# Optimization experiments

Hardware: AMD Instinct MI355X
Metric: run time of the kernel (lower is better)

## Reference

```python
import jax, jax.numpy as jnp
import numpy as np

HIGH, LOW = 768, 384
LOW2 = LOW // 2  # PNL uses low_dim // reduc_ratio, reduc_ratio=2
B, N = 8, 4096
EPS = 1e-5


def _nl_block(x_h, x_l, wg, bg, wt, bt, wp, bp, ww, bw, gamma, beta):
    # x_h: [B,N,H], x_l: [B,N0,H]; conv1x1 == per-token linear
    Nl = x_l.shape[1]
    g = jnp.einsum('bnc,dc->bnd', x_l, wg) + bg      # [B,N0,D]
    th = jnp.einsum('bnc,dc->bnd', x_h, wt) + bt     # [B,N,D]
    ph = jnp.einsum('bnc,dc->bnd', x_l, wp) + bp     # [B,N0,D]
    # attention = (th @ ph^T) / N0; y = attention @ g. Reassociate:
    kv = jnp.einsum('bnd,bne->bde', ph, g) / Nl      # [B,D,D]
    y = jnp.einsum('bnd,bde->bne', th, kv)           # [B,N,D]
    y = jnp.einsum('bnd,cd->bnc', y, ww) + bw        # [B,N,H]
    # BatchNorm1d over channel dim, training-mode batch stats (biased var)
    mu = y.mean(axis=(0, 1))
    var = y.var(axis=(0, 1))
    y = (y - mu) * jax.lax.rsqrt(var + EPS) * gamma + beta
    return y + x_h


def setup_inputs() -> dict:
    key = jax.random.key(0)
    ks = jax.random.split(key, 24)
    s = 0.02
    d = {
        'x': jax.random.normal(ks[0], (B, N, HIGH), jnp.float32),
        'x0': jax.random.normal(ks[1], (B, N, HIGH), jnp.float32),
        # CNL params (low_dim = 384)
        'c_wg': s * jax.random.normal(ks[2], (LOW, HIGH)), 'c_bg': s * jax.random.normal(ks[3], (LOW,)),
        'c_wt': s * jax.random.normal(ks[4], (LOW, HIGH)), 'c_bt': s * jax.random.normal(ks[5], (LOW,)),
        'c_wp': s * jax.random.normal(ks[6], (LOW, HIGH)), 'c_bp': s * jax.random.normal(ks[7], (LOW,)),
        'c_ww': s * jax.random.normal(ks[8], (HIGH, LOW)), 'c_bw': s * jax.random.normal(ks[9], (HIGH,)),
        'c_gamma': 1.0 + 0.1 * jax.random.normal(ks[10], (HIGH,)),
        'c_beta': s * jax.random.normal(ks[11], (HIGH,)),
        # PNL params (low_dim // 2 = 192)
        'p_wg': s * jax.random.normal(ks[12], (LOW2, HIGH)), 'p_bg': s * jax.random.normal(ks[13], (LOW2,)),
        'p_wt': s * jax.random.normal(ks[14], (LOW2, HIGH)), 'p_bt': s * jax.random.normal(ks[15], (LOW2,)),
        'p_wp': s * jax.random.normal(ks[16], (LOW2, HIGH)), 'p_bp': s * jax.random.normal(ks[17], (LOW2,)),
        'p_ww': s * jax.random.normal(ks[18], (HIGH, LOW2)), 'p_bw': s * jax.random.normal(ks[19], (HIGH,)),
        'p_gamma': 1.0 + 0.1 * jax.random.normal(ks[20], (HIGH,)),
        'p_beta': s * jax.random.normal(ks[21], (HIGH,)),
    }
    return d


def reference(x, x0,
              c_wg, c_bg, c_wt, c_bt, c_wp, c_bp, c_ww, c_bw, c_gamma, c_beta,
              p_wg, p_bg, p_wt, p_bt, p_wp, p_bp, p_ww, p_bw, p_gamma, p_beta):
    z = _nl_block(x, x0, c_wg, c_bg, c_wt, c_bt, c_wp, c_bp, c_ww, c_bw, c_gamma, c_beta)
    out = _nl_block(z, x0, p_wg, p_bg, p_wt, p_bt, p_wp, p_bp, p_ww, p_bw, p_gamma, p_beta)
    return out
```

## Files before the change

### kernel.cpp

```cpp
#include <hip/hip_runtime.h>
#include <stdint.h>

typedef unsigned short u16;
typedef __bf16 bf16x8 __attribute__((ext_vector_type(8)));
typedef short s16x8 __attribute__((ext_vector_type(8)));
typedef short s16x4 __attribute__((ext_vector_type(4)));
typedef float f32x4 __attribute__((ext_vector_type(4)));

__device__ __forceinline__ u16 f2bf(float f) {
  uint32_t u = __builtin_bit_cast(uint32_t, f);
  u += 0x7fffu + ((u >> 16) & 1u);
  return (u16)(u >> 16);
}
__device__ __forceinline__ float bf2f(u16 h) {
  uint32_t u = ((uint32_t)h) << 16;
  return __builtin_bit_cast(float, u);
}

__device__ __forceinline__ void gl16(const u16* g, u16* l) {
  __builtin_amdgcn_global_load_lds(
      (const __attribute__((address_space(1))) void*)g,
      (__attribute__((address_space(3))) void*)l, 16, 0, 0);
}

__device__ __forceinline__ void barf() {
  asm volatile("s_barrier" ::: "memory");
}

__device__ __forceinline__ int src_chunk(int l) {
  return (((l & 3) ^ ((l >> 3) & 3)) * 8);
}
__device__ __forceinline__ int rd_koff(int l) {
  return (((l >> 4) ^ (((l & 15) >> 1) & 3)) * 8);
}

__global__ void cvt_in2(const float* __restrict__ a, const float* __restrict__ b,
                        u16* __restrict__ da, u16* __restrict__ db, long n8each) {
  long stride = (long)gridDim.x * blockDim.x;
  long total = 2 * n8each;
  for (long i = (long)blockIdx.x * blockDim.x + threadIdx.x; i < total; i += stride) {
    const float* src = (i < n8each) ? a + i * 8 : b + (i - n8each) * 8;
    u16* dst = (i < n8each) ? da + i * 8 : db + (i - n8each) * 8;
    const f32x4* s = (const f32x4*)src;
    f32x4 v0 = s[0], v1 = s[1];
    s16x8 o;
#pragma unroll
    for (int j = 0; j < 4; ++j) o[j] = (short)f2bf(v0[j]);
#pragma unroll
    for (int j = 0; j < 4; ++j) o[4 + j] = (short)f2bf(v1[j]);
    *(s16x8*)dst = o;
  }
}

__global__ void cvt_flat8(const float* __restrict__ src, u16* __restrict__ dst,
                          long n8, float scale) {
  long stride = (long)gridDim.x * blockDim.x;
  for (long i = (long)blockIdx.x * blockDim.x + threadIdx.x; i < n8; i += stride) {
    const f32x4* s = (const f32x4*)(src + i * 8);
    f32x4 a = s[0], b = s[1];
    s16x8 o;
#pragma unroll
    for (int j = 0; j < 4; ++j) o[j] = (short)f2bf(a[j] * scale);
#pragma unroll
    for (int j = 0; j < 4; ++j) o[4 + j] = (short)f2bf(b[j] * scale);
    *(s16x8*)(dst + i * 8) = o;
  }
}

__global__ void prep_w(const float* __restrict__ c_wg, const float* __restrict__ c_wp,
                       const float* __restrict__ p_wg, const float* __restrict__ p_wp,
                       const float* __restrict__ c_wt, const float* __restrict__ p_wt,
                       const float* __restrict__ c_ww, const float* __restrict__ p_ww,
                       u16* __restrict__ wcat, u16* __restrict__ wt_c,
                       u16* __restrict__ wt_p, u16* __restrict__ ww_c,
                       u16* __restrict__ ww_p) {
  const int C0 = 1280 * 768 / 4;
  const int C1 = C0 + 384 * 768 / 4;
  const int C2 = C1 + 256 * 768 / 4;
  const int C3 = C2 + 768 * 384 / 4;
  const int C4 = C3 + 768 * 256 / 4;
  int stride = gridDim.x * blockDim.x;
  for (int i = blockIdx.x * blockDim.x + threadIdx.x; i < C4; i += stride) {
    const float* src = nullptr;
    u16* dst;
    if (i < C0) {
      int e = i * 4;
      dst = wcat + e;
      int r = e / 768;
      if (r < 384) src = c_wg + e;
      else if (r < 768) src = c_wp + e - 384 * 768;
      else if (r < 960) src = p_wg + e - 768 * 768;
      else if (r < 1024) src = nullptr;
      else if (r < 1216) src = p_wp + e - 1024 * 768;
      else src = nullptr;
    } else if (i < C1) {
      int e = (i - C0) * 4; dst = wt_c + e; src = c_wt + e;
    } else if (i < C2) {
      int e = (i - C1) * 4; dst = wt_p + e;
      src = (e / 768 < 192) ? p_wt + e : nullptr;
    } else if (i < C3) {
      int e = (i - C2) * 4; dst = ww_c + e; src = c_ww + e;
    } else {
      int e = (i - C3) * 4; dst = ww_p + e;
      int r = e >> 8, c = e & 255;
      src = (c < 192) ? p_ww + r * 192 + c : nullptr;
    }
    s16x4 o;
    if (src) {
      f32x4 v = *(const f32x4*)src;
#pragma unroll
      for (int j = 0; j < 4; ++j) o[j] = (short)f2bf(v[j]);
    } else {
      o = s16x4{0, 0, 0, 0};
    }
    *(s16x4*)dst = o;
  }
}

__global__ void prep_b(const float* __restrict__ c_bg, const float* __restrict__ c_bp,
                       const float* __restrict__ p_bg, const float* __restrict__ p_bp,
                       const float* __restrict__ c_bt, const float* __restrict__ p_bt,
                       float* __restrict__ biasb, float* __restrict__ sums) {
  int i = blockIdx.x * blockDim.x + threadIdx.x;
  if (i < 1920) {
    float v = 0.f;
    if (i < 384) v = c_bg[i];
    else if (i < 768) v = c_bp[i - 384];
    else if (i < 960) v = p_bg[i - 768];
    else if (i < 1024) v = 0.f;
    else if (i < 1216) v = p_bp[i - 1024];
    else if (i < 1280) v = 0.f;
    else if (i < 1664) v = c_bt[i - 1280];
    else if (i < 1856) v = p_bt[i - 1664];
    biasb[i] = v;
  } else if (i < 1920 + 24576) {
    sums[i - 1920] = 0.f;
  }
}

template <int BIAS, int SUMS>
__global__ __launch_bounds__(512) void gemm_nt_big(
    const u16* __restrict__ A, const u16* __restrict__ B, void* __restrict__ Cv,
    const float* __restrict__ bias, float* __restrict__ sums,
    int ntiles, long lda, long ldb, long ldc, int K,
    long aBatch, long bBatch, long cBatch) {
  __shared__ u16 As[4][256 * 32];
  __shared__ u16 Bs[4][256 * 32];

  const int bm = blockIdx.x / ntiles;
  const int bn = blockIdx.x % ntiles;
  const int bb = blockIdx.y;
  const int nt = K >> 5;

  const u16* Ab = A + (long)bb * aBatch + (long)bm * 256 * lda;
  const u16* Bb = B + (long)bb * bBatch + (long)bn * 256 * ldb;

  const int t = threadIdx.x;
  const int w = t >> 6;
  const int l = t & 63;
  const int wr = w >> 2;
  const int wc = w & 3;

  const int srow = w * 16 + (l >> 2);
  const int cg = src_chunk(l);
  const long aoff0 = (long)srow * lda + cg;
  const long aoff1 = (long)(128 + srow) * lda + cg;
  const long boff0 = (long)srow * ldb + cg;
  const long boff1 = (long)(128 + srow) * ldb + cg;

#define STAGE_A(T, BUF)                                   \
  gl16(Ab + aoff0 + (long)(T) * 32, &As[BUF][w * 512]);   \
  gl16(Ab + aoff1 + (long)(T) * 32, &As[BUF][(8 + w) * 512]);
#define STAGE_B(T, BUF)                                   \
  gl16(Bb + boff0 + (long)(T) * 32, &Bs[BUF][w * 512]);   \
  gl16(Bb + boff1 + (long)(T) * 32, &Bs[BUF][(8 + w) * 512]);

  f32x4 acc[8][4] = {};

  STAGE_A(0, 0); STAGE_B(0, 0);
  if (nt > 1) { STAGE_A(1, 1); STAGE_B(1, 1); }
  if (nt > 2) { STAGE_A(2, 2); STAGE_B(2, 2); }
  if (nt > 2)      asm volatile("s_waitcnt vmcnt(8)" ::: "memory");
  else if (nt > 1) asm volatile("s_waitcnt vmcnt(4)" ::: "memory");
  else             asm volatile("s_waitcnt vmcnt(0)" ::: "memory");
  barf();

  const int koff = rd_koff(l);
  const int ar = wr * 128 + (l & 15);
  const int br = wc * 64 + (l & 15);

  for (int tt = 0; tt < nt; ++tt) {
    const int cur = tt & 3;
    const int pf = (tt + 3) & 3;
    const bool do_pf = (tt + 3) < nt;

    bf16x8 bfr[4], af[4];
#pragma unroll
    for (int ni = 0; ni < 4; ++ni)
      bfr[ni] = __builtin_bit_cast(
          bf16x8, *(const s16x8*)(&Bs[cur][(br + ni * 16) * 32 + koff]));
#pragma unroll
    for (int mi = 0; mi < 4; ++mi)
      af[mi] = __builtin_bit_cast(
          bf16x8, *(const s16x8*)(&As[cur][(ar + mi * 16) * 32 + koff]));
    if (do_pf) { STAGE_A(tt + 3, pf); }
    barf();
    __builtin_amdgcn_s_setprio(1);
#pragma unroll
    for (int mi = 0; mi < 4; ++mi)
#pragma unroll
      for (int ni = 0; ni < 4; ++ni)
        acc[mi][ni] = __builtin_amdgcn_mfma_f32_16x16x32_bf16(
            af[mi], bfr[ni], acc[mi][ni], 0, 0, 0);
    __builtin_amdgcn_s_setprio(0);
    barf();

    bf16x8 ag[4];
#pragma unroll
    for (int mi = 0; mi < 4; ++mi)
      ag[mi] = __builtin_bit_cast(
          bf16x8, *(const s16x8*)(&As[cur][(ar + 64 + mi * 16) * 32 + koff]));
    if (do_pf) { STAGE_B(tt + 3, pf); }
    barf();
    __builtin_amdgcn_s_setprio(1);
#pragma unroll
    for (int mi = 0; mi < 4; ++mi)
#pragma unroll
      for (int ni = 0; ni < 4; ++ni)
        acc[4 + mi][ni] = __builtin_amdgcn_mfma_f32_16x16x32_bf16(
            ag[mi], bfr[ni], acc[4 + mi][ni], 0, 0, 0);
    __builtin_amdgcn_s_setprio(0);
    if (tt + 4 <= nt)      asm volatile("s_waitcnt vmcnt(8)" ::: "memory");
    else if (tt + 3 == nt) asm volatile("s_waitcnt vmcnt(4)" ::: "memory");
    else if (tt + 2 == nt) asm volatile("s_waitcnt vmcnt(0)" ::: "memory");
    barf();
  }
#undef STAGE_A
#undef STAGE_B
  __builtin_amdgcn_sched_barrier(0);

  const long crow0 = (long)bm * 256 + wr * 128;
  const long ccol0 = (long)bn * 256 + wc * 64;
  u16* C = (u16*)Cv + (long)bb * cBatch;
#pragma unroll
  for (int mi = 0; mi < 8; ++mi)
#pragma unroll
    for (int j = 0; j < 4; ++j) {
      long row = crow0 + mi * 16 + (l >> 4) * 4 + j;
      float rb = (BIAS == 1) ? bias[row] : 0.f;
#pragma unroll
      for (int ni = 0; ni < 4; ++ni) {
        long col = ccol0 + ni * 16 + (l & 15);
        C[row * ldc + col] = f2bf(acc[mi][ni][j] + rb);
      }
    }

  if (SUMS) {
    float* srep = sums + (blockIdx.x & 7) * 1536;
#pragma unroll
    for (int ni = 0; ni < 4; ++ni) {
      float s = 0.f, q = 0.f;
#pragma unroll
      for (int mi = 0; mi < 8; ++mi)
#pragma unroll
        for (int j = 0; j < 4; ++j) {
          float v = acc[mi][ni][j];
          s += v;
          q += v * v;
        }
      s += __shfl_xor(s, 16);
      q += __shfl_xor(q, 16);
      s += __shfl_xor(s, 32);
      q += __shfl_xor(q, 32);
      if (l < 16) {
        long col = ccol0 + ni * 16 + l;
        atomicAdd(&srep[col], s);
        atomicAdd(&srep[768 + col], q);
      }
    }
  }
}

template <int BIAS, int OUT_ATOMIC, int SUMS>
__global__ __launch_bounds__(256) void gemm_nt(
    const u16* __restrict__ A, const u16* __restrict__ B, void* __restrict__ Cv,
    const float* __restrict__ bias, float* __restrict__ sums,
    int ntiles, long lda, long ldb, long ldc, int K,
    long aBatch, long bBatch, long cBatch) {
  __shared__ u16 As[2][128 * 32];
  __shared__ u16 Bs[2][128 * 32];

  const int bm = blockIdx.x / ntiles;
  const int bn = blockIdx.x % ntiles;
  const int bb = blockIdx.y;
  const int kChunk = K / gridDim.z;
  const long k0base = (long)blockIdx.z * kChunk;
  const int nt = kChunk >> 5;

  const u16* Ab = A + (long)bb * aBatch + (long)bm * 128 * lda + k0base;
  const u16* Bb = B + (long)bb * bBatch + (long)bn * 128 * ldb + k0base;

  const int t = threadIdx.x;
  const int w = t >> 6;
  const int l = t & 63;
  const int wr = w >> 1, wc = w & 1;

  const int cg = src_chunk(l);
  const long aoff = (long)(32 * w + (l >> 2)) * lda + cg;
  const long boff = (long)(32 * w + (l >> 2)) * ldb + cg;

  f32x4 acc[4][4] = {};

  gl16(Ab + aoff, &As[0][(32 * w) * 32]);
  gl16(Ab + aoff + 16 * lda, &As[0][(32 * w + 16) * 32]);
  gl16(Bb + boff, &Bs[0][(32 * w) * 32]);
  gl16(Bb + boff + 16 * ldb, &Bs[0][(32 * w + 16) * 32]);
  if (nt > 1) {
    gl16(Ab + aoff + 32, &As[1][(32 * w) * 32]);
    gl16(Ab + aoff + 16 * lda + 32, &As[1][(32 * w + 16) * 32]);
    gl16(Bb + boff + 32, &Bs[1][(32 * w) * 32]);
    gl16(Bb + boff + 16 * ldb + 32, &Bs[1][(32 * w + 16) * 32]);
  }

  const int koff = rd_koff(l);

  for (int tt = 0; tt < nt; ++tt) {
    const int cur = tt & 1;
    if (tt + 1 < nt)
      asm volatile("s_waitcnt vmcnt(4)" ::: "memory");
    else
      asm volatile("s_waitcnt vmcnt(0)" ::: "memory");
    __builtin_amdgcn_s_barrier();

    bf16x8 af[4], bfr[4];
#pragma unroll
    for (int mi = 0; mi < 4; ++mi)
      af[mi] = __builtin_bit_cast(
          bf16x8, *(const s16x8*)(&As[cur][(wr * 64 + mi * 16 + (l & 15)) * 32 + koff]));
#pragma unroll
    for (int ni = 0; ni < 4; ++ni)
      bfr[ni] = __builtin_bit_cast(
          bf16x8, *(const s16x8*)(&Bs[cur][(wc * 64 + ni * 16 + (l & 15)) * 32 + koff]));
#pragma unroll
    for (int mi = 0; mi < 4; ++mi)
#pragma unroll
      for (int ni = 0; ni < 4; ++ni)
        acc[mi][ni] = __builtin_amdgcn_mfma_f32_16x16x32_bf16(
            af[mi], bfr[ni], acc[mi][ni], 0, 0, 0);

    __builtin_amdgcn_s_barrier();
    if (tt + 2 < nt) {
      const long ko = (long)(tt + 2) * 32;
      gl16(Ab + aoff + ko, &As[cur][(32 * w) * 32]);
      gl16(Ab + aoff + 16 * lda + ko, &As[cur][(32 * w + 16) * 32]);
      gl16(Bb + boff + ko, &Bs[cur][(32 * w) * 32]);
      gl16(Bb + boff + 16 * ldb + ko, &Bs[cur][(32 * w + 16) * 32]);
    }
  }
  __builtin_amdgcn_sched_barrier(0);

  const long crow0 = (long)bm * 128 + wr * 64;
  const long ccol0 = (long)bn * 128 + wc * 64;

  if (OUT_ATOMIC) {
    float* C = (float*)Cv + (long)bb * cBatch;
#pragma unroll
    for (int mi = 0; mi < 4; ++mi)
#pragma unroll
      for (int j = 0; j < 4; ++j) {
        long row = crow0 + mi * 16 + (l >> 4) * 4 + j;
#pragma unroll
        for (int ni = 0; ni < 4; ++ni) {
          long col = ccol0 + ni * 16 + (l & 15);
          atomicAdd(&C[row * ldc + col], acc[mi][ni][j]);
        }
      }
  } else {
    u16* C = (u16*)Cv + (long)bb * cBatch;
#pragma unroll
    for (int mi = 0; mi < 4; ++mi)
#pragma unroll
      for (int j = 0; j < 4; ++j) {
        long row = crow0 + mi * 16 + (l >> 4) * 4 + j;
        float rb = (BIAS == 1) ? bias[row] : 0.f;
#pragma unroll
        for (int ni = 0; ni < 4; ++ni) {
          long col = ccol0 + ni * 16 + (l & 15);
          float cb = (BIAS == 2) ? bias[col] : 0.f;
          C[row * ldc + col] = f2bf(acc[mi][ni][j] + rb + cb);
        }
      }
  }

  if (SUMS && !OUT_ATOMIC) {
    float* srep = sums + (blockIdx.x & 7) * 1536;
#pragma unroll
    for (int ni = 0; ni < 4; ++ni) {
      float s = 0.f, q = 0.f;
#pragma unroll
      for (int mi = 0; mi < 4; ++mi)
#pragma unroll
        for (int j = 0; j < 4; ++j) {
          float v = acc[mi][ni][j];
          s += v;
          q += v * v;
        }
      s += __shfl_xor(s, 16);
      q += __shfl_xor(q, 16);
      s += __shfl_xor(s, 32);
      q += __shfl_xor(q, 32);
      if (l < 16) {
        long col = ccol0 + ni * 16 + l;
        atomicAdd(&srep[col], s);
        atomicAdd(&srep[768 + col], q);
      }
    }
  }
}

__global__ void bn_stats(const float* __restrict__ sums, const float* __restrict__ gamma,
                         const float* __restrict__ beta, float* __restrict__ stats,
                         float invN) {
  int c = threadIdx.x;
  float s = 0.f, q = 0.f;
#pragma unroll
  for (int r = 0; r < 8; ++r) {
    s += sums[r * 1536 + c];
    q += sums[r * 1536 + 768 + c];
  }
  float mu = s * invN;
  float var = q * invN - mu * mu;
  float sc = gamma[c] * rsqrtf(var + 1e-5f);
  stats[c] = sc;
  stats[768 + c] = beta[c] - mu * sc;
}

template <int OUT_F32>
__global__ void bn_apply(const u16* __restrict__ pre, const u16* __restrict__ resid,
                         const float* __restrict__ stats, void* __restrict__ out,
                         long n8) {
  long stride = (long)gridDim.x * blockDim.x;
  for (long i = (long)blockIdx.x * blockDim.x + threadIdx.x; i < n8; i += stride) {
    long base = i * 8;
    int c = (int)(base % 768);
    f32x4 sc0 = *(const f32x4*)(stats + c);
    f32x4 sc1 = *(const f32x4*)(stats + c + 4);
    f32x4 sh0 = *(const f32x4*)(stats + 768 + c);
    f32x4 sh1 = *(const f32x4*)(stats + 768 + c + 4);
    s16x8 p = *(const s16x8*)(pre + base);
    s16x8 rv = *(const s16x8*)(resid + base);
    float o[8];
#pragma unroll
    for (int j = 0; j < 4; ++j)
      o[j] = bf2f((u16)p[j]) * sc0[j] + sh0[j] + bf2f((u16)rv[j]);
#pragma unroll
    for (int j = 0; j < 4; ++j)
      o[4 + j] = bf2f((u16)p[4 + j]) * sc1[j] + sh1[j] + bf2f((u16)rv[4 + j]);
    if (OUT_F32) {
      f32x4 o0, o1;
#pragma unroll
      for (int j = 0; j < 4; ++j) { o0[j] = o[j]; o1[j] = o[4 + j]; }
      f32x4* op = (f32x4*)((float*)out + base);
      op[0] = o0;
      op[1] = o1;
    } else {
      s16x8 ov;
#pragma unroll
      for (int j = 0; j < 8; ++j) ov[j] = (short)f2bf(o[j]);
      *(s16x8*)((u16*)out + base) = ov;
    }
  }
}

extern "C" void kernel_launch(void* const* d_in, const int* in_sizes, int n_in,
                              void* d_out, int out_size, void* d_ws, size_t ws_size,
                              hipStream_t stream) {
  const float* x = (const float*)d_in[0];
  const float* x0 = (const float*)d_in[1];
  const float* c_wg = (const float*)d_in[2];
  const float* c_bg = (const float*)d_in[3];
  const float* c_wt = (const float*)d_in[4];
  const float* c_bt = (const float*)d_in[5];
  const float* c_wp = (const float*)d_in[6];
  const float* c_bp = (const float*)d_in[7];
  const float* c_ww = (const float*)d_in[8];
  const float* c_gamma = (const float*)d_in[10];
  const float* c_beta = (const float*)d_in[11];
  const float* p_wg = (const float*)d_in[12];
  const float* p_bg = (const float*)d_in[13];
  const float* p_wt = (const float*)d_in[14];
  const float* p_bt = (const float*)d_in[15];
  const float* p_wp = (const float*)d_in[16];
  const float* p_bp = (const float*)d_in[17];
  const float* p_ww = (const float*)d_in[18];
  const float* p_gamma = (const float*)d_in[20];
  const float* p_beta = (const float*)d_in[21];

  char* ws = (char*)d_ws;
  const long NT = 32768;
  u16* xbf = (u16*)(ws + 0);
  u16* x0bf = (u16*)(ws + 50331648);
  u16* th = (u16*)(ws + 50331648);
  float* kvf_c = (float*)(ws + 75497472);
  float* kvf_p = (float*)(ws + 80216064);
  u16* kvb = (u16*)(ws + 82313216);
  u16* kvwT = (u16*)(ws + 84672512);
  u16* gphT = (u16*)(ws + 100663296);
  u16* wcat = (u16*)(ws + 184549376);
  u16* wt_c = (u16*)(ws + 186515456);
  u16* wt_p = (u16*)(ws + 187105280);
  u16* ww_c = (u16*)(ws + 187498496);
  u16* ww_p = (u16*)(ws + 188088320);
  float* biasb = (float*)(ws + 188481536);
  float* sums = (float*)(ws + 188489216);
  float* stats = (float*)(ws + 188587520);
  u16* zbf = xbf;
  u16* pre = gphT;

  cvt_in2<<<4096, 256, 0, stream>>>(x, x0, xbf, x0bf, NT * 768 / 8);
  prep_w<<<480, 256, 0, stream>>>(c_wg, c_wp, p_wg, p_wp, c_wt, p_wt, c_ww, p_ww,
                                  wcat, wt_c, wt_p, ww_c, ww_p);
  prep_b<<<104, 256, 0, stream>>>(c_bg, c_bp, p_bg, p_bp, c_bt, p_bt, biasb, sums);

  gemm_nt_big<1, 0><<<dim3(5 * 128, 1, 1), 512, 0, stream>>>(
      wcat, x0bf, gphT, biasb, nullptr, 128, 768, 768, 32768, 768, 0, 0, 0);
  hipMemsetAsync(kvf_c, 0, 4718592 + 2097152, stream);

  gemm_nt<2, 0, 0><<<dim3(256 * 3, 1, 1), 256, 0, stream>>>(
      xbf, wt_c, th, biasb + 1280, nullptr, 3, 768, 768, 384, 768, 0, 0, 0);
  gemm_nt<0, 1, 0><<<dim3(9, 8, 4), 256, 0, stream>>>(
      gphT + (long)384 * 32768, gphT, kvf_c, nullptr, nullptr, 3, 32768, 32768,
      384, 4096, 4096, 4096, (long)384 * 384);
  cvt_flat8<<<576, 256, 0, stream>>>(kvf_c, kvb, (long)8 * 384 * 384 / 8, 1.f / 4096.f);
  gemm_nt<0, 0, 0><<<dim3(18, 8, 1), 256, 0, stream>>>(
      ww_c, kvb, kvwT, nullptr, nullptr, 3, 384, 384, 384, 384, 0,
      (long)384 * 384, (long)768 * 384);
  gemm_nt_big<0, 1><<<dim3(48, 8, 1), 512, 0, stream>>>(
      th, kvwT, pre, nullptr, sums, 3, 384, 384, 768, 384, (long)4096 * 384,
      (long)768 * 384, (long)4096 * 768);
  bn_stats<<<1, 768, 0, stream>>>(sums, c_gamma, c_beta, stats, 1.f / 32768.f);
  bn_apply<0><<<2048, 256, 0, stream>>>(pre, xbf, stats, zbf, NT * 768 / 8);

  gemm_nt<2, 0, 0><<<dim3(256 * 2, 1, 1), 256, 0, stream>>>(
      zbf, wt_p, th, biasb + 1664, nullptr, 2, 768, 768, 256, 768, 0, 0, 0);
  gemm_nt<0, 1, 0><<<dim3(4, 8, 8), 256, 0, stream>>>(
      gphT + (long)1024 * 32768, gphT + (long)768 * 32768, kvf_p, nullptr, nullptr,
      2, 32768, 32768, 256, 4096, 4096, 4096, (long)256 * 256);
  cvt_flat8<<<256, 256, 0, stream>>>(kvf_p, kvb, (long)8 * 256 * 256 / 8, 1.f / 4096.f);
  gemm_nt<0, 0, 0><<<dim3(12, 8, 1), 256, 0, stream>>>(
      ww_p, kvb, kvwT, nullptr, nullptr, 2, 256, 256, 256, 192, 0,
      (long)256 * 256, (long)768 * 256);
  gemm_nt_big<0, 1><<<dim3(48, 8, 1), 512, 0, stream>>>(
      th, kvwT, pre, nullptr, sums + 8 * 1536, 3, 256, 256, 768, 192,
      (long)4096 * 256, (long)768 * 256, (long)4096 * 768);
  bn_stats<<<1, 768, 0, stream>>>(sums + 8 * 1536, p_gamma, p_beta, stats, 1.f / 32768.f);
  bn_apply<1><<<2048, 256, 0, stream>>>(pre, zbf, stats, (float*)d_out, NT * 768 / 8);
}
```

Baseline: 434.3 us.

## Restructure big GEMM main loop to 64-wide K tiles with double buffering

The 256x256 GEMM kernel now stages 64-wide K tiles, split into two 32-wide halves, in a two-buffer LDS layout instead of four 32-wide buffers. Each iteration runs four MFMA quadrants, and the loads for the next A and B tiles are interleaved between the quadrants. This halves the number of loop iterations and waitcnt/barrier rounds per K, and raises MFMA work per barrier phase. In exchange it holds more fragment registers live, uses a shallower prefetch depth, and adds more barriers per iteration. It also assumes K is a multiple of 64.

```diff
diff --git a/kernel.cpp b/kernel.cpp
--- a/kernel.cpp
+++ b/kernel.cpp
@@ -144,13 +144,13 @@
     const float* __restrict__ bias, float* __restrict__ sums,
     int ntiles, long lda, long ldb, long ldc, int K,
     long aBatch, long bBatch, long cBatch) {
-  __shared__ u16 As[4][256 * 32];
-  __shared__ u16 Bs[4][256 * 32];
+  __shared__ u16 As[2][2][2][4096];
+  __shared__ u16 Bs[2][2][2][4096];
 
   const int bm = blockIdx.x / ntiles;
   const int bn = blockIdx.x % ntiles;
   const int bb = blockIdx.y;
-  const int nt = K >> 5;
+  const int ntk = K >> 6;
 
   const u16* Ab = A + (long)bb * aBatch + (long)bm * 256 * lda;
   const u16* Bb = B + (long)bb * bBatch + (long)bn * 256 * ldb;
@@ -161,82 +161,118 @@
   const int wr = w >> 2;
   const int wc = w & 3;
 
+  const int cg = src_chunk(l);
   const int srow = w * 16 + (l >> 2);
-  const int cg = src_chunk(l);
-  const long aoff0 = (long)srow * lda + cg;
-  const long aoff1 = (long)(128 + srow) * lda + cg;
-  const long boff0 = (long)srow * ldb + cg;
-  const long boff1 = (long)(128 + srow) * ldb + cg;
-
-#define STAGE_A(T, BUF)                                   \
-  gl16(Ab + aoff0 + (long)(T) * 32, &As[BUF][w * 512]);   \
-  gl16(Ab + aoff1 + (long)(T) * 32, &As[BUF][(8 + w) * 512]);
-#define STAGE_B(T, BUF)                                   \
-  gl16(Bb + boff0 + (long)(T) * 32, &Bs[BUF][w * 512]);   \
-  gl16(Bb + boff1 + (long)(T) * 32, &Bs[BUF][(8 + w) * 512]);
+
+#define ST_A(TK, BUF, H)                                                      \
+  gl16(Ab + (long)((H) * 128 + srow) * lda + (long)(TK) * 64 + cg,            \
+       &As[BUF][H][0][w * 512]);                                              \
+  gl16(Ab + (long)((H) * 128 + srow) * lda + (long)(TK) * 64 + 32 + cg,       \
+       &As[BUF][H][1][w * 512]);
+#define ST_B(TK, BUF, H)                                                      \
+  gl16(Bb + (long)((H) * 128 + srow) * ldb + (long)(TK) * 64 + cg,            \
+       &Bs[BUF][H][0][w * 512]);                                              \
+  gl16(Bb + (long)((H) * 128 + srow) * ldb + (long)(TK) * 64 + 32 + cg,       \
+       &Bs[BUF][H][1][w * 512]);
 
   f32x4 acc[8][4] = {};
 
-  STAGE_A(0, 0); STAGE_B(0, 0);
-  if (nt > 1) { STAGE_A(1, 1); STAGE_B(1, 1); }
-  if (nt > 2) { STAGE_A(2, 2); STAGE_B(2, 2); }
-  if (nt > 2)      asm volatile("s_waitcnt vmcnt(8)" ::: "memory");
-  else if (nt > 1) asm volatile("s_waitcnt vmcnt(4)" ::: "memory");
-  else             asm volatile("s_waitcnt vmcnt(0)" ::: "memory");
-  barf();
-
-  const int koff = rd_koff(l);
-  const int ar = wr * 128 + (l & 15);
-  const int br = wc * 64 + (l & 15);
-
-  for (int tt = 0; tt < nt; ++tt) {
-    const int cur = tt & 3;
-    const int pf = (tt + 3) & 3;
-    const bool do_pf = (tt + 3) < nt;
-
-    bf16x8 bfr[4], af[4];
-#pragma unroll
-    for (int ni = 0; ni < 4; ++ni)
-      bfr[ni] = __builtin_bit_cast(
-          bf16x8, *(const s16x8*)(&Bs[cur][(br + ni * 16) * 32 + koff]));
-#pragma unroll
-    for (int mi = 0; mi < 4; ++mi)
-      af[mi] = __builtin_bit_cast(
-          bf16x8, *(const s16x8*)(&As[cur][(ar + mi * 16) * 32 + koff]));
-    if (do_pf) { STAGE_A(tt + 3, pf); }
+  ST_A(0, 0, 0); ST_A(0, 0, 1);
+  ST_B(0, 0, 0); ST_B(0, 0, 1);
+  if (ntk > 1) { ST_A(1, 1, 0); ST_A(1, 1, 1); }
+
+  const int ko = rd_koff(l);
+  const int rr = l & 15;
+  const int bloc = (wc & 1) * 64;
+
+#define RDA(BUF, KK, MI)                                                       \
+  __builtin_bit_cast(bf16x8, *(const s16x8*)(                                  \
+      &As[BUF][wr][KK][((MI) * 16 + rr) * 32 + ko]))
+#define RDB(BUF, KK, NI)                                                       \
+  __builtin_bit_cast(bf16x8, *(const s16x8*)(                                  \
+      &Bs[BUF][wc >> 1][KK][(bloc + (NI) * 16 + rr) * 32 + ko]))
+
+  for (int kt = 0; kt < ntk; ++kt) {
+    const int b = kt & 1, nb = b ^ 1;
+    const bool h1 = (kt + 1 < ntk), h2 = (kt + 2 < ntk);
+    if (h1) asm volatile("s_waitcnt vmcnt(4)" ::: "memory");
+    else    asm volatile("s_waitcnt vmcnt(0)" ::: "memory");
+    barf();
+
+    bf16x8 a0[4][2], a4[4][2], b0[2][2], b2[2][2];
+
+#pragma unroll
+    for (int mi = 0; mi < 4; ++mi) { a0[mi][0] = RDA(b, 0, mi); a0[mi][1] = RDA(b, 1, mi); }
+#pragma unroll
+    for (int ni = 0; ni < 2; ++ni) { b0[ni][0] = RDB(b, 0, ni); b0[ni][1] = RDB(b, 1, ni); }
+    if (h1) { ST_B(kt + 1, nb, 0); }
     barf();
     __builtin_amdgcn_s_setprio(1);
 #pragma unroll
     for (int mi = 0; mi < 4; ++mi)
 #pragma unroll
-      for (int ni = 0; ni < 4; ++ni)
+      for (int ni = 0; ni < 2; ++ni) {
         acc[mi][ni] = __builtin_amdgcn_mfma_f32_16x16x32_bf16(
-            af[mi], bfr[ni], acc[mi][ni], 0, 0, 0);
+            a0[mi][0], b0[ni][0], acc[mi][ni], 0, 0, 0);
+        acc[mi][ni] = __builtin_amdgcn_mfma_f32_16x16x32_bf16(
+            a0[mi][1], b0[ni][1], acc[mi][ni], 0, 0, 0);
+      }
     __builtin_amdgcn_s_setprio(0);
     barf();
 
-    bf16x8 ag[4];
-#pragma unroll
-    for (int mi = 0; mi < 4; ++mi)
-      ag[mi] = __builtin_bit_cast(
-          bf16x8, *(const s16x8*)(&As[cur][(ar + 64 + mi * 16) * 32 + koff]));
-    if (do_pf) { STAGE_B(tt + 3, pf); }
+#pragma unroll
+    for (int mi = 0; mi < 4; ++mi) { a4[mi][0] = RDA(b, 0, mi + 4); a4[mi][1] = RDA(b, 1, mi + 4); }
+    if (h1) { ST_B(kt + 1, nb, 1); }
     barf();
     __builtin_amdgcn_s_setprio(1);
 #pragma unroll
     for (int mi = 0; mi < 4; ++mi)
 #pragma unroll
-      for (int ni = 0; ni < 4; ++ni)
+      for (int ni = 0; ni < 2; ++ni) {
         acc[4 + mi][ni] = __builtin_amdgcn_mfma_f32_16x16x32_bf16(
-            ag[mi], bfr[ni], acc[4 + mi][ni], 0, 0, 0);
+            a4[mi][0], b0[ni][0], acc[4 + mi][ni], 0, 0, 0);
+        acc[4 + mi][ni] = __builtin_amdgcn_mfma_f32_16x16x32_bf16(
+            a4[mi][1], b0[ni][1], acc[4 + mi][ni], 0, 0, 0);
+      }
     __builtin_amdgcn_s_setprio(0);
-    if (tt + 4 <= nt)      asm volatile("s_waitcnt vmcnt(8)" ::: "memory");
-    else if (tt + 3 == nt) asm volatile("s_waitcnt vmcnt(4)" ::: "memory");
-    else if (tt + 2 == nt) asm volatile("s_waitcnt vmcnt(0)" ::: "memory");
-    barf();
-  }
-#undef STAGE_A
-#undef STAGE_B
+    barf();
+
+#pragma unroll
+    for (int ni = 0; ni < 2; ++ni) { b2[ni][0] = RDB(b, 0, ni + 2); b2[ni][1] = RDB(b, 1, ni + 2); }
+    if (h2) { ST_A(kt + 2, b, 0); }
+    barf();
+    __builtin_amdgcn_s_setprio(1);
+#pragma unroll
+    for (int mi = 0; mi < 4; ++mi)
+#pragma unroll
+      for (int ni = 0; ni < 2; ++ni) {
+        acc[4 + mi][2 + ni] = __builtin_amdgcn_mfma_f32_16x16x32_bf16(
+            a4[mi][0], b2[ni][0], acc[4 + mi][2 + ni], 0, 0, 0);
+        acc[4 + mi][2 + ni] = __builtin_amdgcn_mfma_f32_16x16x32_bf16(
+            a4[mi][1], b2[ni][1], acc[4 + mi][2 + ni], 0, 0, 0);
+      }
+    __builtin_amdgcn_s_setprio(0);
+    barf();
+
+    if (h2) { ST_A(kt + 2, b, 1); }
+    barf();
+    __builtin_amdgcn_s_setprio(1);
+#pragma unroll
+    for (int mi = 0; mi < 4; ++mi)
+#pragma unroll
+      for (int ni = 0; ni < 2; ++ni) {
+        acc[mi][2 + ni] = __builtin_amdgcn_mfma_f32_16x16x32_bf16(
+            a0[mi][0], b2[ni][0], acc[mi][2 + ni], 0, 0, 0);
+        acc[mi][2 + ni] = __builtin_amdgcn_mfma_f32_16x16x32_bf16(
+            a0[mi][1], b2[ni][1], acc[mi][2 + ni], 0, 0, 0);
+      }
+    __builtin_amdgcn_s_setprio(0);
+    barf();
+  }
+#undef ST_A
+#undef ST_B
+#undef RDA
+#undef RDB
   __builtin_amdgcn_sched_barrier(0);
 
   const long crow0 = (long)bm * 256 + wr * 128;
@@ -350,11 +386,11 @@
 
     __builtin_amdgcn_s_barrier();
     if (tt + 2 < nt) {
-      const long ko = (long)(tt + 2) * 32;
-      gl16(Ab + aoff + ko, &As[cur][(32 * w) * 32]);
-      gl16(Ab + aoff + 16 * lda + ko, &As[cur][(32 * w + 16) * 32]);
-      gl16(Bb + boff + ko, &Bs[cur][(32 * w) * 32]);
-      gl16(Bb + boff + 16 * ldb + ko, &Bs[cur][(32 * w + 16) * 32]);
+      const long ko2 = (long)(tt + 2) * 32;
+      gl16(Ab + aoff + ko2, &As[cur][(32 * w) * 32]);
+      gl16(Ab + aoff + 16 * lda + ko2, &As[cur][(32 * w + 16) * 32]);
+      gl16(Bb + boff + ko2, &Bs[cur][(32 * w) * 32]);
+      gl16(Bb + boff + 16 * ldb + ko2, &Bs[cur][(32 * w + 16) * 32]);
     }
   }
   __builtin_amdgcn_sched_barrier(0);
```

New measurement: 419.3 us, median of 2. 1.04x faster.
